# Kernel tuning notes

Measured on AMD Instinct MI355X. Metric: run time of the kernel, lower is better.

## Reference

```python
import jax, jax.numpy as jnp
import numpy as np

N = 100000   # nodes
E = 1600000  # edges
D = 128      # feature dim
DO = 3       # out_head target dim
C = 50000    # centers


def setup_inputs() -> dict:
    key = jax.random.key(0)
    k1, k2, k3, k4 = jax.random.split(key, 4)
    H = jax.random.normal(k1, (N, D), dtype=jnp.float32)
    W = jax.random.normal(k2, (D, DO), dtype=jnp.float32) / np.sqrt(D)
    b = jnp.zeros((DO,), dtype=jnp.float32)
    target = jax.random.normal(k3, (N, DO), dtype=jnp.float32)
    edge_index = jax.random.randint(k4, (2, E), 0, N, dtype=jnp.int32)
    centers = jnp.arange(C, dtype=jnp.int32)  # distinct center node ids
    return {"H": H, "W": W, "b": b, "target": target,
            "edge_index": edge_index, "centers": centers}


def reference(H, W, b, target, edge_index, centers):
    # Vectorized equivalent of the per-center Python loop:
    # for each edge (s, d): if s is a center, pair (owner(s), d) contributes
    # mean-squared error of out_head(H[d]) vs target[d]; then per-center mean,
    # then mean over all centers (empty centers contribute 0 via cnt clamp).
    n_nodes = H.shape[0]
    n_centers = centers.shape[0]
    # node id -> center slot (n_centers == "not a center" sentinel)
    owner_of = jnp.full((n_nodes,), n_centers, dtype=jnp.int32)
    owner_of = owner_of.at[centers].set(jnp.arange(n_centers, dtype=jnp.int32))
    src, dst = edge_index[0], edge_index[1]
    owners = owner_of[src]              # [E]
    mask = owners < n_centers           # [E] edge rooted at a center

    z_frontier = H[dst]                 # [E, D] neighbor-feature gather
    y_hat = z_frontier @ W + b          # [E, DO] out_head (linear)
    y_true = target[dst]                # [E, DO]
    err = jnp.mean((y_hat - y_true) ** 2, axis=-1)  # [E]
    errm = jnp.where(mask, err, jnp.zeros((), err.dtype))

    # segment-mean per center; sentinel bucket n_centers dropped
    loss_sum = jax.ops.segment_sum(errm, owners, num_segments=n_centers + 1)[:n_centers]
    cnt = jax.ops.segment_sum(mask.astype(err.dtype), owners,
                              num_segments=n_centers + 1)[:n_centers]
    aux_loss = jnp.mean(loss_sum / jnp.maximum(cnt, 1.0))
    return aux_loss
```

## Files before the change

### kernel.cpp

```cpp
#include <hip/hip_runtime.h>


#define CNT_SHIFT 44
#define ERR_SCALE 67108864.0f
#define BKT_SHIFT 8
#define BKT_SIZE  256
#define P2B       256
#define ERRB      768
#define BTHR      512
#define STASH     6272
#define PREF_STRIDE 200

__device__ __forceinline__ int owner_fn(int s, bool fast, int C,
                                        const int* __restrict__ arr_idx,
                                        const int* __restrict__ centers) {
    if (fast) return (s < C) ? s : -1;
    int i = arr_idx[s];
    return ((unsigned)i < (unsigned)C && centers[i] == s) ? i : -1;
}

__global__ __launch_bounds__(256)
void prep_kernel(const int* __restrict__ centers,
                 int* __restrict__ arr_idx,
                 int* __restrict__ flagpart,
                 float* __restrict__ out,
                 int C, int out_size) {
    __shared__ int ok;
    int t = threadIdx.x;
    int gtid = blockIdx.x * 256 + t;
    if (t == 0) ok = 1;
    __syncthreads();
    bool mism = false;
    if (gtid < C) {
        int c = centers[gtid];
        arr_idx[c] = gtid;
        mism = (c != gtid);
    }
    if (__ballot(mism) != 0ull && (t & 63) == 0) atomicAnd(&ok, 0);
    __syncthreads();
    if (t == 0) flagpart[blockIdx.x] = ok;
    if (gtid < out_size) out[gtid] = 0.f;
}

__global__ __launch_bounds__(BTHR)
void mid_kernel(const float* __restrict__ H, const float* __restrict__ W,
                const float* __restrict__ b, const float* __restrict__ target,
                const int* __restrict__ eidx, const int* __restrict__ centers,
                const int* __restrict__ arr_idx,
                const int* __restrict__ flagpart,
                float* __restrict__ err_node,
                unsigned short* __restrict__ pref_g,
                unsigned int* __restrict__ pairs,
                int N, int E, int C, int NB, int NBV) {
    __shared__ unsigned int stash[STASH];
    __shared__ unsigned int hist[256];
    __shared__ unsigned int scan[256];
    __shared__ int okflag;
    const int t = threadIdx.x;

    if (blockIdx.x < P2B) {
        if (t == 0) okflag = 1;
        if (t < 256) hist[t] = 0u;
        __syncthreads();
        bool my_ok = (t < NBV) ? (flagpart[t] != 0) : true;
        if (__ballot(!my_ok) != 0ull && (t & 63) == 0) atomicAnd(&okflag, 0);
        __syncthreads();
        const bool fast = (okflag != 0);

        const int E4     = E >> 2;
        const int chunk4 = (E4 + P2B - 1) / P2B;
        const int c0     = blockIdx.x * chunk4;
        const int c1     = min(E4, c0 + chunk4);
        const int4* r0 = reinterpret_cast<const int4*>(eidx);
        const int4* r1 = reinterpret_cast<const int4*>(eidx + E);

        for (int i = c0 + t; i < c1; i += BTHR) {
            int4 s4 = r0[i];
            int ss[4] = {s4.x, s4.y, s4.z, s4.w};
            #pragma unroll
            for (int k = 0; k < 4; ++k) {
                int o = owner_fn(ss[k], fast, C, arr_idx, centers);
                if (o >= 0) atomicAdd(&hist[(unsigned)o >> BKT_SHIFT], 1u);
            }
        }
        __syncthreads();
        if (t < 256) scan[t] = hist[t];
        __syncthreads();
        for (int off = 1; off < 256; off <<= 1) {
            unsigned v = 0;
            if (t < 256 && t >= off) v = scan[t - off];
            __syncthreads();
            if (t < 256 && t >= off) scan[t] += v;
            __syncthreads();
        }
        if (t < 256) {
            unsigned pre = (t == 0) ? 0u : scan[t - 1];
            hist[t] = pre;
            if (t <= NB)
                pref_g[(size_t)blockIdx.x * PREF_STRIDE + t] = (unsigned short)pre;
        }
        __syncthreads();
        for (int i = c0 + t; i < c1; i += BTHR) {
            int4 s4 = r0[i];
            int4 d4 = r1[i];
            int ss[4] = {s4.x, s4.y, s4.z, s4.w};
            int dd[4] = {d4.x, d4.y, d4.z, d4.w};
            #pragma unroll
            for (int k = 0; k < 4; ++k) {
                int o = owner_fn(ss[k], fast, C, arr_idx, centers);
                if (o >= 0) {
                    unsigned bk = (unsigned)o >> BKT_SHIFT;
                    unsigned pos = atomicAdd(&hist[bk], 1u);
                    stash[pos] = (((unsigned)o & (BKT_SIZE - 1)) << 17)
                               | (unsigned)dd[k];
                }
            }
        }
        __syncthreads();
        uint4*       dg = reinterpret_cast<uint4*>(pairs + (size_t)blockIdx.x * STASH);
        const uint4* sg = reinterpret_cast<const uint4*>(stash);
        for (int i = t; i < STASH / 4; i += BTHR) dg[i] = sg[i];
    } else {
        const int lane = t & 63;
        const int sub  = lane >> 5;
        const int l32  = lane & 31;
        float wr[12];
        {
            const float* wb = W + (size_t)(4 * l32) * 3;
            #pragma unroll
            for (int r = 0; r < 12; ++r) wr[r] = wb[r];
        }
        const float b0 = b[0], b1 = b[1], b2 = b[2];
        const float4* H4 = reinterpret_cast<const float4*>(H);
        const int wv    = (blockIdx.x - P2B) * (BTHR >> 6) + (t >> 6);
        const int EW    = ERRB * (BTHR >> 6);
        const int npair = (N + 1) >> 1;
        for (int p = wv; p < npair; p += EW) {
            const int node = 2 * p + sub;
            float4 hv = (node < N) ? H4[(size_t)node * 32 + l32]
                                   : make_float4(0.f, 0.f, 0.f, 0.f);
            float hx[4] = {hv.x, hv.y, hv.z, hv.w};
            float a0 = 0.f, a1 = 0.f, a2 = 0.f;
            #pragma unroll
            for (int r = 0; r < 4; ++r) {
                a0 += hx[r] * wr[r * 3 + 0];
                a1 += hx[r] * wr[r * 3 + 1];
                a2 += hx[r] * wr[r * 3 + 2];
            }
            #pragma unroll
            for (int m = 16; m > 0; m >>= 1) {
                a0 += __shfl_xor(a0, m, 64);
                a1 += __shfl_xor(a1, m, 64);
                a2 += __shfl_xor(a2, m, 64);
            }
            if (l32 == 0 && node < N) {
                float e0 = a0 + b0 - target[(size_t)node * 3 + 0];
                float e1 = a1 + b1 - target[(size_t)node * 3 + 1];
                float e2 = a2 + b2 - target[(size_t)node * 3 + 2];
                err_node[node] = (e0*e0 + e1*e1 + e2*e2) * (1.0f / 3.0f);
            }
        }
    }
}

__global__ __launch_bounds__(256)
void reduce_kernel(const unsigned int* __restrict__ pairs,
                   const unsigned short* __restrict__ pref_g,
                   const float* __restrict__ err_node,
                   float* __restrict__ out, int C, float invC) {
    __shared__ unsigned long long bins[BKT_SIZE];
    __shared__ float wsum[4];
    const int bk = blockIdx.x, t = threadIdx.x;
    bins[t] = 0ull;
    __syncthreads();
    {
        const size_t pb = (size_t)t * PREF_STRIDE;
        unsigned start = pref_g[pb + bk];
        unsigned end   = pref_g[pb + bk + 1];
        const unsigned int* reg = pairs + (size_t)t * STASH;
        for (unsigned i = start; i < end; ++i) {
            unsigned p = reg[i];
            float err = err_node[p & 0x1FFFFu];
            atomicAdd(&bins[p >> 17],
                      (1ull << CNT_SHIFT) + (unsigned long long)(err * ERR_SCALE));
        }
    }
    __syncthreads();
    float term = 0.f;
    {
        int center = bk * BKT_SIZE + t;
        if (center < C) {
            unsigned long long u = bins[t];
            float cnt = (float)(u >> CNT_SHIFT);
            float es  = (float)(u & ((1ull << CNT_SHIFT) - 1)) * (1.0f / ERR_SCALE);
            term = es / fmaxf(cnt, 1.0f);
        }
    }
    #pragma unroll
    for (int m = 32; m > 0; m >>= 1) term += __shfl_down(term, m, 64);
    if ((t & 63) == 0) wsum[t >> 6] = term;
    __syncthreads();
    if (t == 0)
        atomicAdd(out, (wsum[0] + wsum[1] + wsum[2] + wsum[3]) * invC);
}

__global__ __launch_bounds__(256)
void fb_err_kernel(const float* __restrict__ H, const float* __restrict__ W,
                   const float* __restrict__ b, const float* __restrict__ target,
                   const int* __restrict__ centers,
                   float* __restrict__ err_node, int* __restrict__ arr_idx,
                   float* __restrict__ out, int N, int C, int D, int DO,
                   int out_size) {
    int gtid = blockIdx.x * blockDim.x + threadIdx.x;
    if (gtid < C) arr_idx[centers[gtid]] = gtid;
    if (gtid < out_size) out[gtid] = 0.f;
    if (gtid < N) {
        float acc = 0.f;
        for (int j = 0; j < DO; ++j) {
            float a = b[j];
            for (int r = 0; r < D; ++r)
                a += H[(size_t)gtid * D + r] * W[(size_t)r * DO + j];
            float e = a - target[(size_t)gtid * DO + j];
            acc += e * e;
        }
        err_node[gtid] = acc / (float)DO;
    }
}

__global__ void fb_edge_kernel(const int* __restrict__ eidx,
                               const int* __restrict__ arr_idx,
                               const int* __restrict__ centers,
                               const float* __restrict__ err_node,
                               unsigned long long* __restrict__ binsg,
                               int E, int C) {
    int e = blockIdx.x * blockDim.x + threadIdx.x;
    if (e >= E) return;
    int s = eidx[e];
    int o = owner_fn(s, false, C, arr_idx, centers);
    if (o >= 0) {
        int d = eidx[E + e];
        unsigned long long add = (1ull << CNT_SHIFT)
                               + (unsigned long long)(err_node[d] * ERR_SCALE);
        atomicAdd(&binsg[o], add);
    }
}

__global__ void fb_finalize_kernel(const unsigned long long* __restrict__ binsg,
                                   float* __restrict__ out, int C) {
    int i = blockIdx.x * blockDim.x + threadIdx.x;
    float term = 0.f;
    if (i < C) {
        unsigned long long u = binsg[i];
        float cnt = (float)(u >> CNT_SHIFT);
        float es  = (float)(u & ((1ull << CNT_SHIFT) - 1)) * (1.0f / ERR_SCALE);
        term = es / fmaxf(cnt, 1.0f);
    }
    #pragma unroll
    for (int m = 32; m > 0; m >>= 1) term += __shfl_down(term, m, 64);
    __shared__ float wsum[4];
    if ((threadIdx.x & 63) == 0) wsum[threadIdx.x >> 6] = term;
    __syncthreads();
    if (threadIdx.x == 0)
        atomicAdd(out, (wsum[0] + wsum[1] + wsum[2] + wsum[3]) / (float)C);
}

extern "C" void kernel_launch(void* const* d_in, const int* in_sizes, int n_in,
                              void* d_out, int out_size, void* d_ws, size_t ws_size,
                              hipStream_t stream) {
    const float* H      = (const float*)d_in[0];
    const float* W      = (const float*)d_in[1];
    const float* b      = (const float*)d_in[2];
    const float* target = (const float*)d_in[3];
    const int*   eidx   = (const int*)d_in[4];
    const int*   ctrs   = (const int*)d_in[5];

    const int DO = in_sizes[2];
    const int D  = in_sizes[1] / DO;
    const int N  = in_sizes[0] / D;
    const int E  = in_sizes[4] / 2;
    const int C  = in_sizes[5];
    const int NB  = (C + BKT_SIZE - 1) >> BKT_SHIFT;
    const int NBV = (C + 255) / 256;

    size_t off = 0;
    auto take = [&](size_t bytes) {
        void* p = (char*)d_ws + off;
        off = (off + bytes + 255) & ~255ull;
        return p;
    };
    float*          err_node = (float*)take((size_t)N * 4);
    int*            arr_idx  = (int*)take((size_t)N * 4);
    int*            flagpart = (int*)take((size_t)NBV * 4);
    unsigned short* pref_g   = (unsigned short*)take((size_t)P2B * PREF_STRIDE * 2);
    unsigned int*   pairs    = (unsigned int*)((char*)d_ws + off);
    size_t need = off + (size_t)P2B * STASH * 4;

    bool fits = (ws_size >= need) && (NB + 1 <= PREF_STRIDE) && (NBV <= BTHR) &&
                (N < (1 << 17)) && ((E & 3) == 0) && (E <= P2B * STASH) &&
                (D == 128) && (DO == 3);
    if (fits) {
        prep_kernel<<<NBV, 256, 0, stream>>>(ctrs, arr_idx, flagpart,
                                             (float*)d_out, C, out_size);
        mid_kernel<<<P2B + ERRB, BTHR, 0, stream>>>(H, W, b, target, eidx,
                                                    ctrs, arr_idx, flagpart,
                                                    err_node, pref_g, pairs,
                                                    N, E, C, NB, NBV);
        reduce_kernel<<<NB, 256, 0, stream>>>(pairs, pref_g, err_node,
                                              (float*)d_out, C, 1.0f / (float)C);
    } else {
        unsigned long long* binsg = (unsigned long long*)((char*)d_ws + off);
        hipMemsetAsync(binsg, 0, (size_t)C * 8, stream);
        int thr = 256;
        fb_err_kernel<<<(max(N, C) + thr - 1) / thr, thr, 0, stream>>>(
            H, W, b, target, ctrs, err_node, arr_idx, (float*)d_out,
            N, C, D, DO, out_size);
        fb_edge_kernel<<<(E + thr - 1) / thr, thr, 0, stream>>>(
            eidx, arr_idx, ctrs, err_node, binsg, E, C);
        fb_finalize_kernel<<<(C + thr - 1) / thr, thr, 0, stream>>>(
            binsg, (float*)d_out, C);
    }
}
```

Measured before the change: 39.71 us.

## Restructure node-error GEMV into one-node-per-thread LDS-transposed tiles

The per-node error branch of the fused kernel now gives each 256-thread block 256 nodes and assigns one node per thread. H chunks are staged through a transposed, padded LDS tile with register double-buffered loads, and W is read as uniform scalars, which removes the wave-level shuffle reductions. Block size drops from 512 to 256, with the edge-bucketing branch adjusted to match and shared memory unioned between the two roles. The fits check is also tightened to a per-chunk stash bound. The trade-off is a larger grid, many barriers per block, and heavier LDS traffic.

Measured after the change: 41.38 us. 1.04x slower.

```diff
diff --git a/kernel.cpp b/kernel.cpp
--- a/kernel.cpp
+++ b/kernel.cpp
@@ -6,10 +6,10 @@
 #define BKT_SHIFT 8
 #define BKT_SIZE  256
 #define P2B       256
-#define ERRB      768
-#define BTHR      512
+#define BTHR      256
 #define STASH     6272
 #define PREF_STRIDE 200
+#define SMEM_BYTES 32896
 
 __device__ __forceinline__ int owner_fn(int s, bool fast, int C,
                                         const int* __restrict__ arr_idx,
@@ -52,20 +52,21 @@
                 unsigned short* __restrict__ pref_g,
                 unsigned int* __restrict__ pairs,
                 int N, int E, int C, int NB, int NBV) {
-    __shared__ unsigned int stash[STASH];
-    __shared__ unsigned int hist[256];
-    __shared__ unsigned int scan[256];
-    __shared__ int okflag;
+    __shared__ __align__(16) unsigned char smem_raw[SMEM_BYTES];
     const int t = threadIdx.x;
 
     if (blockIdx.x < P2B) {
-        if (t == 0) okflag = 1;
-        if (t < 256) hist[t] = 0u;
+        unsigned int* stash = (unsigned int*)smem_raw;
+        unsigned int* hist  = (unsigned int*)(smem_raw + 25088);
+        unsigned int* scan  = (unsigned int*)(smem_raw + 26112);
+        int*          okf   = (int*)(smem_raw + 27136);
+        if (t == 0) *okf = 1;
+        hist[t] = 0u;
         __syncthreads();
         bool my_ok = (t < NBV) ? (flagpart[t] != 0) : true;
-        if (__ballot(!my_ok) != 0ull && (t & 63) == 0) atomicAnd(&okflag, 0);
-        __syncthreads();
-        const bool fast = (okflag != 0);
+        if (__ballot(!my_ok) != 0ull && (t & 63) == 0) atomicAnd(okf, 0);
+        __syncthreads();
+        const bool fast = (*okf != 0);
 
         const int E4     = E >> 2;
         const int chunk4 = (E4 + P2B - 1) / P2B;
@@ -84,16 +85,15 @@
             }
         }
         __syncthreads();
-        if (t < 256) scan[t] = hist[t];
+        scan[t] = hist[t];
         __syncthreads();
         for (int off = 1; off < 256; off <<= 1) {
-            unsigned v = 0;
-            if (t < 256 && t >= off) v = scan[t - off];
+            unsigned v = (t >= off) ? scan[t - off] : 0u;
             __syncthreads();
-            if (t < 256 && t >= off) scan[t] += v;
+            if (t >= off) scan[t] += v;
             __syncthreads();
         }
-        if (t < 256) {
+        {
             unsigned pre = (t == 0) ? 0u : scan[t - 1];
             hist[t] = pre;
             if (t <= NB)
@@ -121,44 +121,58 @@
         const uint4* sg = reinterpret_cast<const uint4*>(stash);
         for (int i = t; i < STASH / 4; i += BTHR) dg[i] = sg[i];
     } else {
-        const int lane = t & 63;
-        const int sub  = lane >> 5;
-        const int l32  = lane & 31;
-        float wr[12];
-        {
-            const float* wb = W + (size_t)(4 * l32) * 3;
-            #pragma unroll
-            for (int r = 0; r < 12; ++r) wr[r] = wb[r];
-        }
-        const float b0 = b[0], b1 = b[1], b2 = b[2];
-        const float4* H4 = reinterpret_cast<const float4*>(H);
-        const int wv    = (blockIdx.x - P2B) * (BTHR >> 6) + (t >> 6);
-        const int EW    = ERRB * (BTHR >> 6);
-        const int npair = (N + 1) >> 1;
-        for (int p = wv; p < npair; p += EW) {
-            const int node = 2 * p + sub;
-            float4 hv = (node < N) ? H4[(size_t)node * 32 + l32]
-                                   : make_float4(0.f, 0.f, 0.f, 0.f);
-            float hx[4] = {hv.x, hv.y, hv.z, hv.w};
-            float a0 = 0.f, a1 = 0.f, a2 = 0.f;
-            #pragma unroll
-            for (int r = 0; r < 4; ++r) {
-                a0 += hx[r] * wr[r * 3 + 0];
-                a1 += hx[r] * wr[r * 3 + 1];
-                a2 += hx[r] * wr[r * 3 + 2];
-            }
-            #pragma unroll
-            for (int m = 16; m > 0; m >>= 1) {
-                a0 += __shfl_xor(a0, m, 64);
-                a1 += __shfl_xor(a1, m, 64);
-                a2 += __shfl_xor(a2, m, 64);
-            }
-            if (l32 == 0 && node < N) {
-                float e0 = a0 + b0 - target[(size_t)node * 3 + 0];
-                float e1 = a1 + b1 - target[(size_t)node * 3 + 1];
-                float e2 = a2 + b2 - target[(size_t)node * 3 + 2];
-                err_node[node] = (e0*e0 + e1*e1 + e2*e2) * (1.0f / 3.0f);
-            }
+        float* lh = (float*)smem_raw;
+        const int  base  = (blockIdx.x - P2B) * 256;
+        const int  node  = base + t;
+        const bool alive = (node < N);
+        const float4* Hg = reinterpret_cast<const float4*>(H);
+
+        float a0 = 0.f, a1 = 0.f, a2 = 0.f;
+        float4 vA[8], vB[8];
+
+        #define LOADC(c, v)                                                     \
+            { _Pragma("unroll")                                                 \
+              for (int i = 0; i < 8; ++i) {                                     \
+                  int idx = t + 256 * i;                                        \
+                  int row = idx >> 3, q = idx & 7;                              \
+                  int gn = base + row;                                          \
+                  v[i] = (gn < N) ? Hg[(size_t)gn * 32 + (c) * 8 + q]           \
+                                  : make_float4(0.f, 0.f, 0.f, 0.f);            \
+              } }
+        #define WRITEC(v)                                                       \
+            { _Pragma("unroll")                                                 \
+              for (int i = 0; i < 8; ++i) {                                     \
+                  int idx = t + 256 * i;                                        \
+                  int row = idx >> 3, q = idx & 7;                              \
+                  lh[(4 * q + 0) * 257 + row] = v[i].x;                         \
+                  lh[(4 * q + 1) * 257 + row] = v[i].y;                         \
+                  lh[(4 * q + 2) * 257 + row] = v[i].z;                         \
+                  lh[(4 * q + 3) * 257 + row] = v[i].w;                         \
+              } }
+        #define COMPUTEC(c)                                                     \
+            { _Pragma("unroll")                                                 \
+              for (int k = 0; k < 32; ++k) {                                    \
+                  float hk = lh[k * 257 + t];                                   \
+                  a0 += hk * W[((c) * 32 + k) * 3 + 0];                         \
+                  a1 += hk * W[((c) * 32 + k) * 3 + 1];                         \
+                  a2 += hk * W[((c) * 32 + k) * 3 + 2];                         \
+              } }
+
+        LOADC(0, vA)
+        __syncthreads(); WRITEC(vA) __syncthreads(); LOADC(1, vB) COMPUTEC(0)
+        __syncthreads(); WRITEC(vB) __syncthreads(); LOADC(2, vA) COMPUTEC(1)
+        __syncthreads(); WRITEC(vA) __syncthreads(); LOADC(3, vB) COMPUTEC(2)
+        __syncthreads(); WRITEC(vB) __syncthreads();              COMPUTEC(3)
+
+        #undef LOADC
+        #undef WRITEC
+        #undef COMPUTEC
+
+        if (alive) {
+            float e0 = a0 + b[0] - target[(size_t)node * 3 + 0];
+            float e1 = a1 + b[1] - target[(size_t)node * 3 + 1];
+            float e2 = a2 + b[2] - target[(size_t)node * 3 + 2];
+            err_node[node] = (e0 * e0 + e1 * e1 + e2 * e2) * (1.0f / 3.0f);
         }
     }
 }
@@ -281,6 +295,7 @@
     const int C  = in_sizes[5];
     const int NB  = (C + BKT_SIZE - 1) >> BKT_SHIFT;
     const int NBV = (C + 255) / 256;
+    const int NERRB = (N + 255) / 256;
 
     size_t off = 0;
     auto take = [&](size_t bytes) {
@@ -295,16 +310,17 @@
     unsigned int*   pairs    = (unsigned int*)((char*)d_ws + off);
     size_t need = off + (size_t)P2B * STASH * 4;
 
+    int chunk_edges = 4 * ((E / 4 + P2B - 1) / P2B);
     bool fits = (ws_size >= need) && (NB + 1 <= PREF_STRIDE) && (NBV <= BTHR) &&
-                (N < (1 << 17)) && ((E & 3) == 0) && (E <= P2B * STASH) &&
+                (N < (1 << 17)) && ((E & 3) == 0) && (chunk_edges <= STASH) &&
                 (D == 128) && (DO == 3);
     if (fits) {
         prep_kernel<<<NBV, 256, 0, stream>>>(ctrs, arr_idx, flagpart,
                                              (float*)d_out, C, out_size);
-        mid_kernel<<<P2B + ERRB, BTHR, 0, stream>>>(H, W, b, target, eidx,
-                                                    ctrs, arr_idx, flagpart,
-                                                    err_node, pref_g, pairs,
-                                                    N, E, C, NB, NBV);
+        mid_kernel<<<P2B + NERRB, BTHR, 0, stream>>>(H, W, b, target, eidx,
+                                                     ctrs, arr_idx, flagpart,
+                                                     err_node, pref_g, pairs,
+                                                     N, E, C, NB, NBV);
         reduce_kernel<<<NB, 256, 0, stream>>>(pairs, pref_g, err_node,
                                               (float*)d_out, C, 1.0f / (float)C);
     } else {
```

## Widen reduce blocks, trim stash copy, replace output atomics with final kernel

Applied to the files above, without the earlier changes.

The reduce kernel now runs 1024 threads per bucket block, with four threads splitting each source segment so the per-center accumulation gets more parallelism. Each block writes a partial sum, and a new single-block final kernel combines them, replacing the float atomicAdd on the output. The stash copy-out writes only the filled entries instead of the full stash, and the error-computation block count drops from 768 to 512. The cost is an extra kernel launch, and running fewer error blocks could lengthen that part of the work.

New measurement: 35.16 us. -11.5%, faster.

```diff
diff --git a/kernel.cpp b/kernel.cpp
--- a/kernel.cpp
+++ b/kernel.cpp
@@ -6,7 +6,7 @@
 #define BKT_SHIFT 8
 #define BKT_SIZE  256
 #define P2B       256
-#define ERRB      768
+#define ERRB      512
 #define BTHR      512
 #define STASH     6272
 #define PREF_STRIDE 200
@@ -39,7 +39,7 @@
     if (__ballot(mism) != 0ull && (t & 63) == 0) atomicAnd(&ok, 0);
     __syncthreads();
     if (t == 0) flagpart[blockIdx.x] = ok;
-    if (gtid < out_size) out[gtid] = 0.f;
+    if (gtid >= 1 && gtid < out_size) out[gtid] = 0.f;
 }
 
 __global__ __launch_bounds__(BTHR)
@@ -55,17 +55,18 @@
     __shared__ unsigned int stash[STASH];
     __shared__ unsigned int hist[256];
     __shared__ unsigned int scan[256];
-    __shared__ int okflag;
+    __shared__ unsigned int total_sh;
+    __shared__ int okf;
     const int t = threadIdx.x;
 
     if (blockIdx.x < P2B) {
-        if (t == 0) okflag = 1;
+        if (t == 0) okf = 1;
         if (t < 256) hist[t] = 0u;
         __syncthreads();
         bool my_ok = (t < NBV) ? (flagpart[t] != 0) : true;
-        if (__ballot(!my_ok) != 0ull && (t & 63) == 0) atomicAnd(&okflag, 0);
-        __syncthreads();
-        const bool fast = (okflag != 0);
+        if (__ballot(!my_ok) != 0ull && (t & 63) == 0) atomicAnd(&okf, 0);
+        __syncthreads();
+        const bool fast = (okf != 0);
 
         const int E4     = E >> 2;
         const int chunk4 = (E4 + P2B - 1) / P2B;
@@ -87,8 +88,7 @@
         if (t < 256) scan[t] = hist[t];
         __syncthreads();
         for (int off = 1; off < 256; off <<= 1) {
-            unsigned v = 0;
-            if (t < 256 && t >= off) v = scan[t - off];
+            unsigned v = (t < 256 && t >= off) ? scan[t - off] : 0u;
             __syncthreads();
             if (t < 256 && t >= off) scan[t] += v;
             __syncthreads();
@@ -99,6 +99,7 @@
             if (t <= NB)
                 pref_g[(size_t)blockIdx.x * PREF_STRIDE + t] = (unsigned short)pre;
         }
+        if (t == 0) total_sh = scan[255];
         __syncthreads();
         for (int i = c0 + t; i < c1; i += BTHR) {
             int4 s4 = r0[i];
@@ -117,13 +118,14 @@
             }
         }
         __syncthreads();
-        uint4*       dg = reinterpret_cast<uint4*>(pairs + (size_t)blockIdx.x * STASH);
-        const uint4* sg = reinterpret_cast<const uint4*>(stash);
-        for (int i = t; i < STASH / 4; i += BTHR) dg[i] = sg[i];
+        {
+            unsigned nvec = (total_sh + 3u) >> 2;
+            uint4*       dg = reinterpret_cast<uint4*>(pairs + (size_t)blockIdx.x * STASH);
+            const uint4* sg = reinterpret_cast<const uint4*>(stash);
+            for (unsigned i = t; i < nvec; i += BTHR) dg[i] = sg[i];
+        }
     } else {
-        const int lane = t & 63;
-        const int sub  = lane >> 5;
-        const int l32  = lane & 31;
+        const int lane = t & 63, sub = lane >> 5, l32 = lane & 31;
         float wr[12];
         {
             const float* wb = W + (size_t)(4 * l32) * 3;
@@ -163,22 +165,24 @@
     }
 }
 
-__global__ __launch_bounds__(256)
+__global__ __launch_bounds__(1024)
 void reduce_kernel(const unsigned int* __restrict__ pairs,
                    const unsigned short* __restrict__ pref_g,
                    const float* __restrict__ err_node,
-                   float* __restrict__ out, int C, float invC) {
+                   float* __restrict__ partial, int C) {
     __shared__ unsigned long long bins[BKT_SIZE];
-    __shared__ float wsum[4];
+    __shared__ float wsum[16];
     const int bk = blockIdx.x, t = threadIdx.x;
-    bins[t] = 0ull;
+    if (t < BKT_SIZE) bins[t] = 0ull;
     __syncthreads();
     {
-        const size_t pb = (size_t)t * PREF_STRIDE;
+        const int seg = t >> 2;
+        const int j   = t & 3;
+        const size_t pb = (size_t)seg * PREF_STRIDE;
         unsigned start = pref_g[pb + bk];
         unsigned end   = pref_g[pb + bk + 1];
-        const unsigned int* reg = pairs + (size_t)t * STASH;
-        for (unsigned i = start; i < end; ++i) {
+        const unsigned int* reg = pairs + (size_t)seg * STASH;
+        for (unsigned i = start + j; i < end; i += 4) {
             unsigned p = reg[i];
             float err = err_node[p & 0x1FFFFu];
             atomicAdd(&bins[p >> 17],
@@ -187,7 +191,7 @@
     }
     __syncthreads();
     float term = 0.f;
-    {
+    if (t < BKT_SIZE) {
         int center = bk * BKT_SIZE + t;
         if (center < C) {
             unsigned long long u = bins[t];
@@ -200,8 +204,25 @@
     for (int m = 32; m > 0; m >>= 1) term += __shfl_down(term, m, 64);
     if ((t & 63) == 0) wsum[t >> 6] = term;
     __syncthreads();
-    if (t == 0)
-        atomicAdd(out, (wsum[0] + wsum[1] + wsum[2] + wsum[3]) * invC);
+    if (t == 0) {
+        float s = 0.f;
+        #pragma unroll
+        for (int w = 0; w < 16; ++w) s += wsum[w];
+        partial[bk] = s;
+    }
+}
+
+__global__ __launch_bounds__(256)
+void final_kernel(const float* __restrict__ partial,
+                  float* __restrict__ out, int NB, float invC) {
+    __shared__ float wsum[4];
+    const int t = threadIdx.x;
+    float v = (t < NB) ? partial[t] : 0.f;
+    #pragma unroll
+    for (int m = 32; m > 0; m >>= 1) v += __shfl_down(v, m, 64);
+    if ((t & 63) == 0) wsum[t >> 6] = v;
+    __syncthreads();
+    if (t == 0) out[0] = (wsum[0] + wsum[1] + wsum[2] + wsum[3]) * invC;
 }
 
 __global__ __launch_bounds__(256)
@@ -292,12 +313,14 @@
     int*            arr_idx  = (int*)take((size_t)N * 4);
     int*            flagpart = (int*)take((size_t)NBV * 4);
     unsigned short* pref_g   = (unsigned short*)take((size_t)P2B * PREF_STRIDE * 2);
+    float*          partial  = (float*)take((size_t)NB * 4);
     unsigned int*   pairs    = (unsigned int*)((char*)d_ws + off);
     size_t need = off + (size_t)P2B * STASH * 4;
 
+    int chunk_edges = 4 * ((E / 4 + P2B - 1) / P2B);
     bool fits = (ws_size >= need) && (NB + 1 <= PREF_STRIDE) && (NBV <= BTHR) &&
-                (N < (1 << 17)) && ((E & 3) == 0) && (E <= P2B * STASH) &&
-                (D == 128) && (DO == 3);
+                (N < (1 << 17)) && ((E & 3) == 0) && (chunk_edges <= STASH) &&
+                (D == 128) && (DO == 3) && (out_size >= 1);
     if (fits) {
         prep_kernel<<<NBV, 256, 0, stream>>>(ctrs, arr_idx, flagpart,
                                              (float*)d_out, C, out_size);
@@ -305,8 +328,10 @@
                                                     ctrs, arr_idx, flagpart,
                                                     err_node, pref_g, pairs,
                                                     N, E, C, NB, NBV);
-        reduce_kernel<<<NB, 256, 0, stream>>>(pairs, pref_g, err_node,
-                                              (float*)d_out, C, 1.0f / (float)C);
+        reduce_kernel<<<NB, 1024, 0, stream>>>(pairs, pref_g, err_node,
+                                               partial, C);
+        final_kernel<<<1, 256, 0, stream>>>(partial, (float*)d_out, NB,
+                                            1.0f / (float)C);
     } else {
         unsigned long long* binsg = (unsigned long long*)((char*)d_ws + off);
         hipMemsetAsync(binsg, 0, (size_t)C * 8, stream);
```
